# Performance work log

Measured on AMD Instinct MI355X. Metric: run time of the kernel, lower is better.

## Reference

```python
import jax, jax.numpy as jnp
import numpy as np

B, N = 8, 512
EMBED, EDGE_D, FLAG_D = 256, 32, 32
NODE_NUM, EDGE_NUM, FLAG_NUM = 20000, 16, 4
IN_DIM = 2 * EMBED + 2 * FLAG_D + EDGE_D  # concat order: [head_emb, tail_emb, head_flag, tail_flag, edge]
NEG = -1e12


def setup_inputs() -> dict:
    key = jax.random.key(0)
    ks = jax.random.split(key, 16)
    s = 0.05
    return {
        "adjacent_matrix": jax.random.randint(ks[0], (B, N, N), 0, 2, dtype=jnp.int32),
        "head_nodes": jax.random.randint(ks[1], (B, N), 0, NODE_NUM, dtype=jnp.int32),
        "head_flag_bit_matrix": jax.random.randint(ks[2], (B, N), 0, FLAG_NUM, dtype=jnp.int32),
        "edge_type_matrix": jax.random.randint(ks[3], (B, N, N), 0, EDGE_NUM, dtype=jnp.int32),
        "node_emb": jax.random.normal(ks[4], (NODE_NUM, EMBED)) * s,
        "edge_emb": jax.random.normal(ks[5], (EDGE_NUM, EDGE_D)) * s,
        "flag_emb": jax.random.normal(ks[6], (FLAG_NUM, FLAG_D)) * s,
        "t1_w": jax.random.normal(ks[7], (EMBED, EMBED)) * s,
        "t1_b": jax.random.normal(ks[8], (EMBED,)) * s,
        "w1": jax.random.normal(ks[9], (IN_DIM,)) * s,
        "b1": jax.random.normal(ks[10], ()) * s,
        "t2_w": jax.random.normal(ks[11], (EMBED, EMBED)) * s,
        "t2_b": jax.random.normal(ks[12], (EMBED,)) * s,
        "w2": jax.random.normal(ks[13], (IN_DIM,)) * s,
        "b2": jax.random.normal(ks[14], ()) * s,
    }


def _leaky_relu(x):
    return jnp.where(x > 0, x, 0.1 * x)


def _gat_layer(h, f, e, adj, w, b):
    # Decompose Linear(concat([h_i, h_j, f_i, f_j, e_ij])) into per-part dot
    # products summed by broadcasting -> avoids the [B,N,N,IN_DIM] concat.
    D, F = h.shape[-1], f.shape[-1]
    wh, wt = w[:D], w[D:2 * D]
    wfh, wft = w[2 * D:2 * D + F], w[2 * D + F:2 * D + 2 * F]
    we = w[2 * D + 2 * F:]
    logit = ((h @ wh)[:, :, None] + (h @ wt)[:, None, :]
             + (f @ wfh)[:, :, None] + (f @ wft)[:, None, :]
             + jnp.einsum('bije,e->bij', e, we) + b)  # [B,N,N]
    logit = _leaky_relu(logit)
    logit = jnp.where(adj == 0, NEG, logit)
    att = jax.nn.softmax(logit, axis=1)  # softmax over head axis i
    # out[b,j] = sum_i att[b,i,j] * h[b,i]   (== bmm(att^T, h))
    return jnp.einsum('bij,bid->bjd', att, h)


def reference(adjacent_matrix, head_nodes, head_flag_bit_matrix, edge_type_matrix,
              node_emb, edge_emb, flag_emb,
              t1_w, t1_b, w1, b1, t2_w, t2_b, w2, b2):
    h = node_emb[head_nodes] @ t1_w.T + t1_b          # [B,N,D] (t1 projection)
    f = flag_emb[head_flag_bit_matrix]                # [B,N,F]
    e = edge_emb[edge_type_matrix]                    # [B,N,N,E]
    t = _gat_layer(h, f, e, adjacent_matrix, w1, b1)  # layer 1 aggregate
    t = jax.nn.sigmoid(t)
    h2 = t @ t2_w.T + t2_b                            # t2 projection
    return _gat_layer(h2, f, e, adjacent_matrix, w2, b2)
```

## Files before the change

### kernel.cpp

```cpp
#include <hip/hip_runtime.h>
#include <hip/hip_bf16.h>

#define BB 8
#define NN 512
#define DD 256
#define NROWS (BB*NN)
#define JT 16

using bf16x8 = __attribute__((ext_vector_type(8))) short;
using f32x4  = __attribute__((ext_vector_type(4))) float;
typedef unsigned short us_t;

__device__ __forceinline__ us_t f2bf(float x) {
    union { float f; unsigned int u; } v; v.f = x;
    unsigned int r = (v.u + 0x7fffu + ((v.u >> 16) & 1u)) >> 16;
    return (us_t)r;
}

__global__ __launch_bounds__(256) void k1(
    const float* __restrict__ w1f, const float* __restrict__ bias1,
    const float* __restrict__ node_emb, const int* __restrict__ head_nodes,
    const float* __restrict__ wvec1, const int* __restrict__ flagidx,
    const float* __restrict__ flag_emb,
    us_t* __restrict__ hT, float* __restrict__ a1, float* __restrict__ c1,
    const float* __restrict__ w2f, us_t* __restrict__ Wb2,
    const int* __restrict__ adj, const int* __restrict__ et,
    unsigned char* __restrict__ pk)
{
    __shared__ float redA[64], redC[64];
    const int blk = blockIdx.x, t = threadIdx.x;

    if (blk >= 320) {
        int pb = blk - 320;
        int pbid = ((pb & 7) << 8) | (pb >> 3);
        int g = (pbid*256 + t)*4;
        int4 av = *(const int4*)(adj + g);
        int4 ev = *(const int4*)(et + g);
        uchar4 u;
        u.x = (unsigned char)((ev.x&15)|(av.x<<4));
        u.y = (unsigned char)((ev.y&15)|(av.y<<4));
        u.z = (unsigned char)((ev.z&15)|(av.z<<4));
        u.w = (unsigned char)((ev.w&15)|(av.w<<4));
        *(uchar4*)(pk + g) = u;
        return;
    }
    if (blk >= 256) {
        int i = (blk - 256)*1024 + t*4;
        float4 wv = *(const float4*)(w2f + i);
        ushort4 u;
        u.x = f2bf(wv.x); u.y = f2bf(wv.y); u.z = f2bf(wv.z); u.w = f2bf(wv.w);
        *(ushort4*)&Wb2[i] = u;
        return;
    }

    const int bid = ((blk & 7) << 5) | (blk >> 3);
    const int wave = t >> 6, lane = t & 63;
    const int lrow = lane & 15, kg = lane >> 4;
    const int r0 = bid * 16;
    const int dw = wave * 64;

    const int arow = r0 + lrow;
    const int nid = head_nodes[arow];

    f32x4 acc[4];
    #pragma unroll
    for (int n = 0; n < 4; ++n) acc[n] = (f32x4){0.f, 0.f, 0.f, 0.f};

    const float4* xr = (const float4*)(node_emb + (size_t)nid * DD);
    #pragma unroll
    for (int ks = 0; ks < DD/32; ++ks) {
        float4 xa = xr[ks*8 + kg*2];
        float4 xb = xr[ks*8 + kg*2 + 1];
        bf16x8 af;
        af[0] = (short)f2bf(xa.x); af[1] = (short)f2bf(xa.y);
        af[2] = (short)f2bf(xa.z); af[3] = (short)f2bf(xa.w);
        af[4] = (short)f2bf(xb.x); af[5] = (short)f2bf(xb.y);
        af[6] = (short)f2bf(xb.z); af[7] = (short)f2bf(xb.w);
        #pragma unroll
        for (int n = 0; n < 4; ++n) {
            const float4* wr = (const float4*)(w1f + (size_t)(dw + n*16 + lrow)*DD
                                                + ks*32 + kg*8);
            float4 wa = wr[0], wb = wr[1];
            bf16x8 bfr;
            bfr[0] = (short)f2bf(wa.x); bfr[1] = (short)f2bf(wa.y);
            bfr[2] = (short)f2bf(wa.z); bfr[3] = (short)f2bf(wa.w);
            bfr[4] = (short)f2bf(wb.x); bfr[5] = (short)f2bf(wb.y);
            bfr[6] = (short)f2bf(wb.z); bfr[7] = (short)f2bf(wb.w);
            acc[n] = __builtin_amdgcn_mfma_f32_16x16x32_bf16(af, bfr, acc[n], 0, 0, 0);
        }
    }

    const int b  = r0 >> 9;
    const int i0 = (r0 & 511) + kg*4;
    float pa[4] = {0.f,0.f,0.f,0.f}, pc[4] = {0.f,0.f,0.f,0.f};
    #pragma unroll
    for (int n = 0; n < 4; ++n) {
        int d = dw + n*16 + lrow;
        float bv = bias1[d];
        float whd = wvec1[d], wtd = wvec1[256+d];
        ushort4 u;
        #pragma unroll
        for (int r = 0; r < 4; ++r) {
            float v = acc[n][r] + bv;
            ((us_t*)&u)[r] = f2bf(v);
            pa[r] += v * whd;
            pc[r] += v * wtd;
        }
        *(ushort4*)&hT[(size_t)b*DD*NN + (size_t)d*NN + i0] = u;
    }
    #pragma unroll
    for (int r = 0; r < 4; ++r) {
        #pragma unroll
        for (int m = 1; m < 16; m <<= 1) {
            pa[r] += __shfl_xor(pa[r], m);
            pc[r] += __shfl_xor(pc[r], m);
        }
    }
    if (lrow == 0) {
        #pragma unroll
        for (int r = 0; r < 4; ++r) {
            redA[wave*16 + kg*4 + r] = pa[r];
            redC[wave*16 + kg*4 + r] = pc[r];
        }
    }
    __syncthreads();
    if (t < 128) {
        const int m = t >> 3, sub = t & 7;
        const int fi = flagidx[r0 + m];
        float fa = 0.f, fc = 0.f;
        #pragma unroll
        for (int q = 0; q < 4; ++q) {
            int e = sub*4 + q;
            float fe = flag_emb[fi*32 + e];
            fa += fe * wvec1[512 + e];
            fc += fe * wvec1[544 + e];
        }
        #pragma unroll
        for (int mm = 1; mm < 8; mm <<= 1) {
            fa += __shfl_xor(fa, mm);
            fc += __shfl_xor(fc, mm);
        }
        if (sub == 0) {
            float sa = fa, sc = fc;
            #pragma unroll
            for (int wv = 0; wv < 4; ++wv) { sa += redA[wv*16 + m]; sc += redC[wv*16 + m]; }
            a1[r0 + m] = sa;
            c1[r0 + m] = sc;
        }
    }
}

__global__ __launch_bounds__(512) void attn1_lin2(
    const unsigned char* __restrict__ pk,
    const float* __restrict__ edge_emb, const float* __restrict__ w,
    const float* __restrict__ bptr,
    const float* __restrict__ a, const float* __restrict__ c,
    const us_t* __restrict__ hT,
    const us_t* __restrict__ Wb2, const float* __restrict__ bias2,
    const float* __restrict__ wvec2, const int* __restrict__ flagidx,
    const float* __restrict__ flag_emb,
    us_t* __restrict__ hT2, float* __restrict__ a2, float* __restrict__ c2)
{
    __shared__ __align__(16) float p[NN][JT+1];
    __shared__ __align__(16) us_t Pb[JT][NN+8];
    __shared__ __align__(16) us_t Sg[16][DD+8];
    __shared__ float as[NN];
    __shared__ float edot[16];
    __shared__ float cjs[JT];
    __shared__ float redw[8][16];
    __shared__ float mj[JT];
    __shared__ float invden[JT];
    __shared__ float redA[128], redC[128];

    const int t = threadIdx.x;
    const int b  = blockIdx.x & 7;
    const int j0 = (blockIdx.x >> 3) * JT;
    const int wave = t >> 6, lane = t & 63;

    as[t] = a[b*NN + t];
    if (t < 16) {
        float s = 0.f;
        for (int e2 = 0; e2 < 32; ++e2)
            s += edge_emb[t*32 + e2] * w[576 + e2];
        edot[t] = s;
    } else if (t < 32) {
        cjs[t-16] = c[b*NN + j0 + (t-16)];
    }
    const float bias = bptr[0];
    __syncthreads();

    const unsigned char* pkb = pk + (size_t)b*NN*NN + j0;
    #pragma unroll
    for (int it = 0; it < 4; ++it) {
        int lid4 = (it*512 + t) * 4;
        int i = lid4 >> 4, jj = lid4 & 15;
        uchar4 u = *(const uchar4*)(pkb + (size_t)i*NN + jj);
        float base = as[i] + bias;
        unsigned char uv[4] = {u.x, u.y, u.z, u.w};
        #pragma unroll
        for (int q = 0; q < 4; ++q) {
            float l = base + cjs[jj+q] + edot[uv[q] & 15];
            l = (l > 0.f) ? l : 0.1f*l;
            p[i][jj+q] = (uv[q] >> 4) ? l : -1.0e30f;
        }
    }
    __syncthreads();

    const int j = t & 15, grp = t >> 4;
    float lv[16];
    #pragma unroll
    for (int s = 0; s < 16; ++s) lv[s] = p[grp + s*32][j];
    float m = lv[0];
    #pragma unroll
    for (int s = 1; s < 16; ++s) m = fmaxf(m, lv[s]);
    m = fmaxf(m, __shfl_xor(m, 16));
    m = fmaxf(m, __shfl_xor(m, 32));
    if (lane < 16) redw[wave][lane] = m;
    __syncthreads();
    if (t < 16) {
        float mm = redw[0][t];
        #pragma unroll
        for (int wv = 1; wv < 8; ++wv) mm = fmaxf(mm, redw[wv][t]);
        mj[t] = mm;
    }
    __syncthreads();
    const float mmax = mj[j];
    float ssum = 0.f;
    #pragma unroll
    for (int s = 0; s < 16; ++s) {
        float v = __expf(lv[s] - mmax);
        Pb[j][grp + s*32] = f2bf(v);
        ssum += v;
    }
    ssum += __shfl_xor(ssum, 16);
    ssum += __shfl_xor(ssum, 32);
    if (lane < 16) redw[wave][lane] = ssum;
    __syncthreads();
    if (t < 16) {
        float sm = redw[0][t];
        #pragma unroll
        for (int wv = 1; wv < 8; ++wv) sm += redw[wv][t];
        invden[t] = 1.f / sm;
    }
    __syncthreads();

    const int dw = wave * 32;
    const int lrow = lane & 15;
    const int kg   = lane >> 4;
    f32x4 acc[2];
    acc[0] = (f32x4){0.f,0.f,0.f,0.f};
    acc[1] = (f32x4){0.f,0.f,0.f,0.f};

    const us_t* hTb = hT + (size_t)b*DD*NN;
    const us_t* hp[2];
    hp[0] = hTb + (size_t)(dw + lrow)*NN + kg*8;
    hp[1] = hTb + (size_t)(dw + 16 + lrow)*NN + kg*8;

    #pragma unroll 4
    for (int ks = 0; ks < NN/32; ++ks) {
        int k0 = ks*32;
        bf16x8 afr = *(const bf16x8*)&Pb[lrow][kg*8 + k0];
        #pragma unroll
        for (int n = 0; n < 2; ++n) {
            bf16x8 bfr = *(const bf16x8*)(hp[n] + k0);
            acc[n] = __builtin_amdgcn_mfma_f32_16x16x32_bf16(afr, bfr, acc[n], 0, 0, 0);
        }
    }

    float idr[4];
    #pragma unroll
    for (int r = 0; r < 4; ++r) idr[r] = invden[kg*4 + r];
    #pragma unroll
    for (int n = 0; n < 2; ++n) {
        #pragma unroll
        for (int r = 0; r < 4; ++r) {
            float v = 1.f/(1.f + __expf(-acc[n][r]*idr[r]));
            Sg[kg*4 + r][dw + n*16 + lrow] = f2bf(v);
        }
    }
    __syncthreads();

    f32x4 acc2[2];
    acc2[0] = (f32x4){0.f,0.f,0.f,0.f};
    acc2[1] = (f32x4){0.f,0.f,0.f,0.f};
    #pragma unroll
    for (int ks = 0; ks < DD/32; ++ks) {
        bf16x8 af2 = *(const bf16x8*)&Sg[lrow][ks*32 + kg*8];
        #pragma unroll
        for (int n = 0; n < 2; ++n) {
            bf16x8 bf2 = *(const bf16x8*)(Wb2 + (size_t)(dw + n*16 + lrow)*DD
                                           + ks*32 + kg*8);
            acc2[n] = __builtin_amdgcn_mfma_f32_16x16x32_bf16(af2, bf2, acc2[n], 0, 0, 0);
        }
    }

    const int r0 = b*NN + j0;
    const int i0 = j0 + kg*4;
    float pa[4] = {0.f,0.f,0.f,0.f}, pc[4] = {0.f,0.f,0.f,0.f};
    #pragma unroll
    for (int n = 0; n < 2; ++n) {
        int d = dw + n*16 + lrow;
        float bv = bias2[d];
        float whd = wvec2[d], wtd = wvec2[256+d];
        ushort4 u;
        #pragma unroll
        for (int r = 0; r < 4; ++r) {
            float v = acc2[n][r] + bv;
            ((us_t*)&u)[r] = f2bf(v);
            pa[r] += v * whd;
            pc[r] += v * wtd;
        }
        *(ushort4*)&hT2[(size_t)b*DD*NN + (size_t)d*NN + i0] = u;
    }
    #pragma unroll
    for (int r = 0; r < 4; ++r) {
        #pragma unroll
        for (int mk = 1; mk < 16; mk <<= 1) {
            pa[r] += __shfl_xor(pa[r], mk);
            pc[r] += __shfl_xor(pc[r], mk);
        }
    }
    if (lrow == 0) {
        #pragma unroll
        for (int r = 0; r < 4; ++r) {
            redA[wave*16 + kg*4 + r] = pa[r];
            redC[wave*16 + kg*4 + r] = pc[r];
        }
    }
    __syncthreads();
    if (t < 128) {
        const int mrow = t >> 3, sub = t & 7;
        const int fi = flagidx[r0 + mrow];
        float fa = 0.f, fc = 0.f;
        #pragma unroll
        for (int q = 0; q < 4; ++q) {
            int e = sub*4 + q;
            float fe = flag_emb[fi*32 + e];
            fa += fe * wvec2[512 + e];
            fc += fe * wvec2[544 + e];
        }
        #pragma unroll
        for (int mm = 1; mm < 8; mm <<= 1) {
            fa += __shfl_xor(fa, mm);
            fc += __shfl_xor(fc, mm);
        }
        if (sub == 0) {
            float sa = fa, sc = fc;
            #pragma unroll
            for (int wv = 0; wv < 8; ++wv) { sa += redA[wv*16 + mrow]; sc += redC[wv*16 + mrow]; }
            a2[r0 + mrow] = sa;
            c2[r0 + mrow] = sc;
        }
    }
}

__global__ __launch_bounds__(512) void attn2(
    const unsigned char* __restrict__ pk,
    const float* __restrict__ edge_emb, const float* __restrict__ w,
    const float* __restrict__ bptr,
    const float* __restrict__ a, const float* __restrict__ c,
    const us_t* __restrict__ hT,
    float* __restrict__ outf)
{
    __shared__ __align__(16) float p[NN][JT+1];
    __shared__ __align__(16) us_t Pb[JT][NN+8];
    __shared__ float as[NN];
    __shared__ float edot[16];
    __shared__ float cjs[JT];
    __shared__ float redw[8][16];
    __shared__ float mj[JT];
    __shared__ float invden[JT];

    const int t = threadIdx.x;
    const int b  = blockIdx.x & 7;
    const int j0 = (blockIdx.x >> 3) * JT;
    const int wave = t >> 6, lane = t & 63;

    as[t] = a[b*NN + t];
    if (t < 16) {
        float s = 0.f;
        for (int e2 = 0; e2 < 32; ++e2)
            s += edge_emb[t*32 + e2] * w[576 + e2];
        edot[t] = s;
    } else if (t < 32) {
        cjs[t-16] = c[b*NN + j0 + (t-16)];
    }
    const float bias = bptr[0];
    __syncthreads();

    const unsigned char* pkb = pk + (size_t)b*NN*NN + j0;
    #pragma unroll
    for (int it = 0; it < 4; ++it) {
        int lid4 = (it*512 + t) * 4;
        int i = lid4 >> 4, jj = lid4 & 15;
        uchar4 u = *(const uchar4*)(pkb + (size_t)i*NN + jj);
        float base = as[i] + bias;
        unsigned char uv[4] = {u.x, u.y, u.z, u.w};
        #pragma unroll
        for (int q = 0; q < 4; ++q) {
            float l = base + cjs[jj+q] + edot[uv[q] & 15];
            l = (l > 0.f) ? l : 0.1f*l;
            p[i][jj+q] = (uv[q] >> 4) ? l : -1.0e30f;
        }
    }
    __syncthreads();

    const int j = t & 15, grp = t >> 4;
    float lv[16];
    #pragma unroll
    for (int s = 0; s < 16; ++s) lv[s] = p[grp + s*32][j];
    float m = lv[0];
    #pragma unroll
    for (int s = 1; s < 16; ++s) m = fmaxf(m, lv[s]);
    m = fmaxf(m, __shfl_xor(m, 16));
    m = fmaxf(m, __shfl_xor(m, 32));
    if (lane < 16) redw[wave][lane] = m;
    __syncthreads();
    if (t < 16) {
        float mm = redw[0][t];
        #pragma unroll
        for (int wv = 1; wv < 8; ++wv) mm = fmaxf(mm, redw[wv][t]);
        mj[t] = mm;
    }
    __syncthreads();
    const float mmax = mj[j];
    float ssum = 0.f;
    #pragma unroll
    for (int s = 0; s < 16; ++s) {
        float v = __expf(lv[s] - mmax);
        Pb[j][grp + s*32] = f2bf(v);
        ssum += v;
    }
    ssum += __shfl_xor(ssum, 16);
    ssum += __shfl_xor(ssum, 32);
    if (lane < 16) redw[wave][lane] = ssum;
    __syncthreads();
    if (t < 16) {
        float sm = redw[0][t];
        #pragma unroll
        for (int wv = 1; wv < 8; ++wv) sm += redw[wv][t];
        invden[t] = 1.f / sm;
    }
    __syncthreads();

    const int dw = wave * 32;
    const int lrow = lane & 15;
    const int kg   = lane >> 4;
    f32x4 acc[2];
    acc[0] = (f32x4){0.f,0.f,0.f,0.f};
    acc[1] = (f32x4){0.f,0.f,0.f,0.f};

    const us_t* hTb = hT + (size_t)b*DD*NN;
    const us_t* hp[2];
    hp[0] = hTb + (size_t)(dw + lrow)*NN + kg*8;
    hp[1] = hTb + (size_t)(dw + 16 + lrow)*NN + kg*8;

    #pragma unroll 4
    for (int ks = 0; ks < NN/32; ++ks) {
        int k0 = ks*32;
        bf16x8 afr = *(const bf16x8*)&Pb[lrow][kg*8 + k0];
        #pragma unroll
        for (int n = 0; n < 2; ++n) {
            bf16x8 bfr = *(const bf16x8*)(hp[n] + k0);
            acc[n] = __builtin_amdgcn_mfma_f32_16x16x32_bf16(afr, bfr, acc[n], 0, 0, 0);
        }
    }

    float idr[4];
    #pragma unroll
    for (int r = 0; r < 4; ++r) idr[r] = invden[kg*4 + r];
    #pragma unroll
    for (int n = 0; n < 2; ++n) {
        #pragma unroll
        for (int r = 0; r < 4; ++r) {
            int jj = j0 + kg*4 + r;
            int dd = dw + n*16 + lrow;
            outf[(size_t)(b*NN + jj)*DD + dd] = acc[n][r] * idr[r];
        }
    }
}

extern "C" void kernel_launch(void* const* d_in, const int* in_sizes, int n_in,
                              void* d_out, int out_size, void* d_ws, size_t ws_size,
                              hipStream_t stream) {
    (void)in_sizes; (void)n_in; (void)out_size; (void)ws_size;
    const int*   adj       = (const int*)d_in[0];
    const int*   head_nodes= (const int*)d_in[1];
    const int*   head_flag = (const int*)d_in[2];
    const int*   etype     = (const int*)d_in[3];
    const float* node_emb  = (const float*)d_in[4];
    const float* edge_emb  = (const float*)d_in[5];
    const float* flag_emb  = (const float*)d_in[6];
    const float* t1_w      = (const float*)d_in[7];
    const float* t1_b      = (const float*)d_in[8];
    const float* w1        = (const float*)d_in[9];
    const float* b1        = (const float*)d_in[10];
    const float* t2_w      = (const float*)d_in[11];
    const float* t2_b      = (const float*)d_in[12];
    const float* w2        = (const float*)d_in[13];
    const float* b2        = (const float*)d_in[14];

    us_t* hT1 = (us_t*)d_ws;
    us_t* hT2 = hT1 + (size_t)NROWS*DD;
    us_t* Wb2 = hT2 + (size_t)NROWS*DD;
    unsigned char* pk = (unsigned char*)(Wb2 + (size_t)DD*DD);
    float* a1 = (float*)(pk + (size_t)BB*NN*NN);
    float* c1 = a1 + NROWS;
    float* a2 = c1 + NROWS;
    float* c2 = a2 + NROWS;

    k1<<<320 + BB*NN*NN/1024, 256, 0, stream>>>(
        t1_w, t1_b, node_emb, head_nodes, w1, head_flag, flag_emb,
        hT1, a1, c1, t2_w, Wb2, adj, etype, pk);
    attn1_lin2<<<BB*(NN/JT), 512, 0, stream>>>(
        pk, edge_emb, w1, b1, a1, c1, hT1,
        Wb2, t2_b, w2, head_flag, flag_emb, hT2, a2, c2);
    attn2<<<BB*(NN/JT), 512, 0, stream>>>(
        pk, edge_emb, w2, b2, a2, c2, hT2, (float*)d_out);
}
```

Measured before the change: 46.35 us.

## Fuse both attention layers into one cooperative kernel with per-batch barrier

Merges the two attention kernels into a single cooperatively launched kernel. Blocks of the same batch synchronize through an atomic counter that k1 zeroes, replacing the kernel boundary between layer 1 and layer 2. This removes one launch gap and its tail, at the cost of spin-waiting and the need for all 256 blocks to be co-resident.

```diff
diff --git a/kernel.cpp b/kernel.cpp
--- a/kernel.cpp
+++ b/kernel.cpp
@@ -25,7 +25,7 @@
     us_t* __restrict__ hT, float* __restrict__ a1, float* __restrict__ c1,
     const float* __restrict__ w2f, us_t* __restrict__ Wb2,
     const int* __restrict__ adj, const int* __restrict__ et,
-    unsigned char* __restrict__ pk)
+    unsigned char* __restrict__ pk, int* __restrict__ ctr)
 {
     __shared__ float redA[64], redC[64];
     const int blk = blockIdx.x, t = threadIdx.x;
@@ -45,6 +45,7 @@
         return;
     }
     if (blk >= 256) {
+        if (blk == 256 && t < BB) ctr[t] = 0;
         int i = (blk - 256)*1024 + t*4;
         float4 wv = *(const float4*)(w2f + i);
         ushort4 u;
@@ -150,16 +151,20 @@
     }
 }
 
-__global__ __launch_bounds__(512) void attn1_lin2(
-    const unsigned char* __restrict__ pk,
-    const float* __restrict__ edge_emb, const float* __restrict__ w,
-    const float* __restrict__ bptr,
-    const float* __restrict__ a, const float* __restrict__ c,
-    const us_t* __restrict__ hT,
-    const us_t* __restrict__ Wb2, const float* __restrict__ bias2,
-    const float* __restrict__ wvec2, const int* __restrict__ flagidx,
-    const float* __restrict__ flag_emb,
-    us_t* __restrict__ hT2, float* __restrict__ a2, float* __restrict__ c2)
+struct AttnParams {
+    const unsigned char* pk;
+    const float *edge_emb;
+    const float *w1, *b1, *a1, *c1;
+    const us_t  *hT1;
+    const us_t  *Wb2; const float *bias2;
+    const float *w2;  const int *flagidx; const float *flag_emb;
+    us_t *hT2; float *a2; float *c2;
+    const float *b2;
+    float *outf;
+    int *ctr;
+};
+
+__global__ __launch_bounds__(512) void attn_fused(AttnParams P)
 {
     __shared__ __align__(16) float p[NN][JT+1];
     __shared__ __align__(16) us_t Pb[JT][NN+8];
@@ -176,306 +181,295 @@
     const int b  = blockIdx.x & 7;
     const int j0 = (blockIdx.x >> 3) * JT;
     const int wave = t >> 6, lane = t & 63;
-
-    as[t] = a[b*NN + t];
-    if (t < 16) {
-        float s = 0.f;
-        for (int e2 = 0; e2 < 32; ++e2)
-            s += edge_emb[t*32 + e2] * w[576 + e2];
-        edot[t] = s;
-    } else if (t < 32) {
-        cjs[t-16] = c[b*NN + j0 + (t-16)];
-    }
-    const float bias = bptr[0];
+    const int lrow = lane & 15, kg = lane >> 4;
+
+    {
+        as[t] = P.a1[b*NN + t];
+        if (t < 16) {
+            float s = 0.f;
+            for (int e2 = 0; e2 < 32; ++e2)
+                s += P.edge_emb[t*32 + e2] * P.w1[576 + e2];
+            edot[t] = s;
+        } else if (t < 32) {
+            cjs[t-16] = P.c1[b*NN + j0 + (t-16)];
+        }
+        const float bias = P.b1[0];
+        __syncthreads();
+
+        const unsigned char* pkb = P.pk + (size_t)b*NN*NN + j0;
+        #pragma unroll
+        for (int it = 0; it < 4; ++it) {
+            int lid4 = (it*512 + t) * 4;
+            int i = lid4 >> 4, jj = lid4 & 15;
+            uchar4 u = *(const uchar4*)(pkb + (size_t)i*NN + jj);
+            float base = as[i] + bias;
+            unsigned char uv[4] = {u.x, u.y, u.z, u.w};
+            #pragma unroll
+            for (int q = 0; q < 4; ++q) {
+                float l = base + cjs[jj+q] + edot[uv[q] & 15];
+                l = (l > 0.f) ? l : 0.1f*l;
+                p[i][jj+q] = (uv[q] >> 4) ? l : -1.0e30f;
+            }
+        }
+        __syncthreads();
+
+        const int j = t & 15, grp = t >> 4;
+        float lv[16];
+        #pragma unroll
+        for (int s = 0; s < 16; ++s) lv[s] = p[grp + s*32][j];
+        float m = lv[0];
+        #pragma unroll
+        for (int s = 1; s < 16; ++s) m = fmaxf(m, lv[s]);
+        m = fmaxf(m, __shfl_xor(m, 16));
+        m = fmaxf(m, __shfl_xor(m, 32));
+        if (lane < 16) redw[wave][lane] = m;
+        __syncthreads();
+        if (t < 16) {
+            float mm = redw[0][t];
+            #pragma unroll
+            for (int wv = 1; wv < 8; ++wv) mm = fmaxf(mm, redw[wv][t]);
+            mj[t] = mm;
+        }
+        __syncthreads();
+        const float mmax = mj[j];
+        float ssum = 0.f;
+        #pragma unroll
+        for (int s = 0; s < 16; ++s) {
+            float v = __expf(lv[s] - mmax);
+            Pb[j][grp + s*32] = f2bf(v);
+            ssum += v;
+        }
+        ssum += __shfl_xor(ssum, 16);
+        ssum += __shfl_xor(ssum, 32);
+        if (lane < 16) redw[wave][lane] = ssum;
+        __syncthreads();
+        if (t < 16) {
+            float sm = redw[0][t];
+            #pragma unroll
+            for (int wv = 1; wv < 8; ++wv) sm += redw[wv][t];
+            invden[t] = 1.f / sm;
+        }
+        __syncthreads();
+
+        const int dw = wave * 32;
+        f32x4 acc[2];
+        acc[0] = (f32x4){0.f,0.f,0.f,0.f};
+        acc[1] = (f32x4){0.f,0.f,0.f,0.f};
+
+        const us_t* hTb = P.hT1 + (size_t)b*DD*NN;
+        const us_t* hp[2];
+        hp[0] = hTb + (size_t)(dw + lrow)*NN + kg*8;
+        hp[1] = hTb + (size_t)(dw + 16 + lrow)*NN + kg*8;
+
+        #pragma unroll 4
+        for (int ks = 0; ks < NN/32; ++ks) {
+            int k0 = ks*32;
+            bf16x8 afr = *(const bf16x8*)&Pb[lrow][kg*8 + k0];
+            #pragma unroll
+            for (int n = 0; n < 2; ++n) {
+                bf16x8 bfr = *(const bf16x8*)(hp[n] + k0);
+                acc[n] = __builtin_amdgcn_mfma_f32_16x16x32_bf16(afr, bfr, acc[n], 0, 0, 0);
+            }
+        }
+
+        float idr[4];
+        #pragma unroll
+        for (int r = 0; r < 4; ++r) idr[r] = invden[kg*4 + r];
+        #pragma unroll
+        for (int n = 0; n < 2; ++n) {
+            #pragma unroll
+            for (int r = 0; r < 4; ++r) {
+                float v = 1.f/(1.f + __expf(-acc[n][r]*idr[r]));
+                Sg[kg*4 + r][dw + n*16 + lrow] = f2bf(v);
+            }
+        }
+        __syncthreads();
+
+        f32x4 acc2[2];
+        acc2[0] = (f32x4){0.f,0.f,0.f,0.f};
+        acc2[1] = (f32x4){0.f,0.f,0.f,0.f};
+        #pragma unroll
+        for (int ks = 0; ks < DD/32; ++ks) {
+            bf16x8 af2 = *(const bf16x8*)&Sg[lrow][ks*32 + kg*8];
+            #pragma unroll
+            for (int n = 0; n < 2; ++n) {
+                bf16x8 bf2 = *(const bf16x8*)(P.Wb2 + (size_t)(dw + n*16 + lrow)*DD
+                                               + ks*32 + kg*8);
+                acc2[n] = __builtin_amdgcn_mfma_f32_16x16x32_bf16(af2, bf2, acc2[n], 0, 0, 0);
+            }
+        }
+
+        const int r0 = b*NN + j0;
+        const int i0 = j0 + kg*4;
+        float pa[4] = {0.f,0.f,0.f,0.f}, pc[4] = {0.f,0.f,0.f,0.f};
+        #pragma unroll
+        for (int n = 0; n < 2; ++n) {
+            int d = dw + n*16 + lrow;
+            float bv = P.bias2[d];
+            float whd = P.w2[d], wtd = P.w2[256+d];
+            ushort4 u;
+            #pragma unroll
+            for (int r = 0; r < 4; ++r) {
+                float v = acc2[n][r] + bv;
+                ((us_t*)&u)[r] = f2bf(v);
+                pa[r] += v * whd;
+                pc[r] += v * wtd;
+            }
+            *(ushort4*)&P.hT2[(size_t)b*DD*NN + (size_t)d*NN + i0] = u;
+        }
+        #pragma unroll
+        for (int r = 0; r < 4; ++r) {
+            #pragma unroll
+            for (int mk = 1; mk < 16; mk <<= 1) {
+                pa[r] += __shfl_xor(pa[r], mk);
+                pc[r] += __shfl_xor(pc[r], mk);
+            }
+        }
+        if (lrow == 0) {
+            #pragma unroll
+            for (int r = 0; r < 4; ++r) {
+                redA[wave*16 + kg*4 + r] = pa[r];
+                redC[wave*16 + kg*4 + r] = pc[r];
+            }
+        }
+        __syncthreads();
+        if (t < 128) {
+            const int mrow = t >> 3, sub = t & 7;
+            const int fi = P.flagidx[r0 + mrow];
+            float fa = 0.f, fc = 0.f;
+            #pragma unroll
+            for (int q = 0; q < 4; ++q) {
+                int e = sub*4 + q;
+                float fe = P.flag_emb[fi*32 + e];
+                fa += fe * P.w2[512 + e];
+                fc += fe * P.w2[544 + e];
+            }
+            #pragma unroll
+            for (int mm = 1; mm < 8; mm <<= 1) {
+                fa += __shfl_xor(fa, mm);
+                fc += __shfl_xor(fc, mm);
+            }
+            if (sub == 0) {
+                float sa = fa, sc = fc;
+                #pragma unroll
+                for (int wv = 0; wv < 8; ++wv) { sa += redA[wv*16 + mrow]; sc += redC[wv*16 + mrow]; }
+                P.a2[r0 + mrow] = sa;
+                P.c2[r0 + mrow] = sc;
+            }
+        }
+    }
+
     __syncthreads();
-
-    const unsigned char* pkb = pk + (size_t)b*NN*NN + j0;
-    #pragma unroll
-    for (int it = 0; it < 4; ++it) {
-        int lid4 = (it*512 + t) * 4;
-        int i = lid4 >> 4, jj = lid4 & 15;
-        uchar4 u = *(const uchar4*)(pkb + (size_t)i*NN + jj);
-        float base = as[i] + bias;
-        unsigned char uv[4] = {u.x, u.y, u.z, u.w};
-        #pragma unroll
-        for (int q = 0; q < 4; ++q) {
-            float l = base + cjs[jj+q] + edot[uv[q] & 15];
-            l = (l > 0.f) ? l : 0.1f*l;
-            p[i][jj+q] = (uv[q] >> 4) ? l : -1.0e30f;
-        }
-    }
+    __threadfence();
     __syncthreads();
-
-    const int j = t & 15, grp = t >> 4;
-    float lv[16];
-    #pragma unroll
-    for (int s = 0; s < 16; ++s) lv[s] = p[grp + s*32][j];
-    float m = lv[0];
-    #pragma unroll
-    for (int s = 1; s < 16; ++s) m = fmaxf(m, lv[s]);
-    m = fmaxf(m, __shfl_xor(m, 16));
-    m = fmaxf(m, __shfl_xor(m, 32));
-    if (lane < 16) redw[wave][lane] = m;
+    if (t == 0) {
+        atomicAdd(P.ctr + b, 1);
+        while (__hip_atomic_load(P.ctr + b, __ATOMIC_ACQUIRE,
+                                 __HIP_MEMORY_SCOPE_AGENT) < 32) {}
+    }
     __syncthreads();
-    if (t < 16) {
-        float mm = redw[0][t];
-        #pragma unroll
-        for (int wv = 1; wv < 8; ++wv) mm = fmaxf(mm, redw[wv][t]);
-        mj[t] = mm;
-    }
-    __syncthreads();
-    const float mmax = mj[j];
-    float ssum = 0.f;
-    #pragma unroll
-    for (int s = 0; s < 16; ++s) {
-        float v = __expf(lv[s] - mmax);
-        Pb[j][grp + s*32] = f2bf(v);
-        ssum += v;
-    }
-    ssum += __shfl_xor(ssum, 16);
-    ssum += __shfl_xor(ssum, 32);
-    if (lane < 16) redw[wave][lane] = ssum;
-    __syncthreads();
-    if (t < 16) {
-        float sm = redw[0][t];
-        #pragma unroll
-        for (int wv = 1; wv < 8; ++wv) sm += redw[wv][t];
-        invden[t] = 1.f / sm;
-    }
-    __syncthreads();
-
-    const int dw = wave * 32;
-    const int lrow = lane & 15;
-    const int kg   = lane >> 4;
-    f32x4 acc[2];
-    acc[0] = (f32x4){0.f,0.f,0.f,0.f};
-    acc[1] = (f32x4){0.f,0.f,0.f,0.f};
-
-    const us_t* hTb = hT + (size_t)b*DD*NN;
-    const us_t* hp[2];
-    hp[0] = hTb + (size_t)(dw + lrow)*NN + kg*8;
-    hp[1] = hTb + (size_t)(dw + 16 + lrow)*NN + kg*8;
-
-    #pragma unroll 4
-    for (int ks = 0; ks < NN/32; ++ks) {
-        int k0 = ks*32;
-        bf16x8 afr = *(const bf16x8*)&Pb[lrow][kg*8 + k0];
+    __threadfence();
+
+    {
+        as[t] = P.a2[b*NN + t];
+        if (t < 16) {
+            float s = 0.f;
+            for (int e2 = 0; e2 < 32; ++e2)
+                s += P.edge_emb[t*32 + e2] * P.w2[576 + e2];
+            edot[t] = s;
+        } else if (t < 32) {
+            cjs[t-16] = P.c2[b*NN + j0 + (t-16)];
+        }
+        const float bias = P.b2[0];
+        __syncthreads();
+
+        const unsigned char* pkb = P.pk + (size_t)b*NN*NN + j0;
+        #pragma unroll
+        for (int it = 0; it < 4; ++it) {
+            int lid4 = (it*512 + t) * 4;
+            int i = lid4 >> 4, jj = lid4 & 15;
+            uchar4 u = *(const uchar4*)(pkb + (size_t)i*NN + jj);
+            float base = as[i] + bias;
+            unsigned char uv[4] = {u.x, u.y, u.z, u.w};
+            #pragma unroll
+            for (int q = 0; q < 4; ++q) {
+                float l = base + cjs[jj+q] + edot[uv[q] & 15];
+                l = (l > 0.f) ? l : 0.1f*l;
+                p[i][jj+q] = (uv[q] >> 4) ? l : -1.0e30f;
+            }
+        }
+        __syncthreads();
+
+        const int j = t & 15, grp = t >> 4;
+        float lv[16];
+        #pragma unroll
+        for (int s = 0; s < 16; ++s) lv[s] = p[grp + s*32][j];
+        float m = lv[0];
+        #pragma unroll
+        for (int s = 1; s < 16; ++s) m = fmaxf(m, lv[s]);
+        m = fmaxf(m, __shfl_xor(m, 16));
+        m = fmaxf(m, __shfl_xor(m, 32));
+        if (lane < 16) redw[wave][lane] = m;
+        __syncthreads();
+        if (t < 16) {
+            float mm = redw[0][t];
+            #pragma unroll
+            for (int wv = 1; wv < 8; ++wv) mm = fmaxf(mm, redw[wv][t]);
+            mj[t] = mm;
+        }
+        __syncthreads();
+        const float mmax = mj[j];
+        float ssum = 0.f;
+        #pragma unroll
+        for (int s = 0; s < 16; ++s) {
+            float v = __expf(lv[s] - mmax);
+            Pb[j][grp + s*32] = f2bf(v);
+            ssum += v;
+        }
+        ssum += __shfl_xor(ssum, 16);
+        ssum += __shfl_xor(ssum, 32);
+        if (lane < 16) redw[wave][lane] = ssum;
+        __syncthreads();
+        if (t < 16) {
+            float sm = redw[0][t];
+            #pragma unroll
+            for (int wv = 1; wv < 8; ++wv) sm += redw[wv][t];
+            invden[t] = 1.f / sm;
+        }
+        __syncthreads();
+
+        const int dw = wave * 32;
+        f32x4 acc[2];
+        acc[0] = (f32x4){0.f,0.f,0.f,0.f};
+        acc[1] = (f32x4){0.f,0.f,0.f,0.f};
+
+        const us_t* hTb = P.hT2 + (size_t)b*DD*NN;
+        const us_t* hp[2];
+        hp[0] = hTb + (size_t)(dw + lrow)*NN + kg*8;
+        hp[1] = hTb + (size_t)(dw + 16 + lrow)*NN + kg*8;
+
+        #pragma unroll 4
+        for (int ks = 0; ks < NN/32; ++ks) {
+            int k0 = ks*32;
+            bf16x8 afr = *(const bf16x8*)&Pb[lrow][kg*8 + k0];
+            #pragma unroll
+            for (int n = 0; n < 2; ++n) {
+                bf16x8 bfr = *(const bf16x8*)(hp[n] + k0);
+                acc[n] = __builtin_amdgcn_mfma_f32_16x16x32_bf16(afr, bfr, acc[n], 0, 0, 0);
+            }
+        }
+
+        float idr[4];
+        #pragma unroll
+        for (int r = 0; r < 4; ++r) idr[r] = invden[kg*4 + r];
         #pragma unroll
         for (int n = 0; n < 2; ++n) {
-            bf16x8 bfr = *(const bf16x8*)(hp[n] + k0);
-            acc[n] = __builtin_amdgcn_mfma_f32_16x16x32_bf16(afr, bfr, acc[n], 0, 0, 0);
-        }
-    }
-
-    float idr[4];
-    #pragma unroll
-    for (int r = 0; r < 4; ++r) idr[r] = invden[kg*4 + r];
-    #pragma unroll
-    for (int n = 0; n < 2; ++n) {
-        #pragma unroll
-        for (int r = 0; r < 4; ++r) {
-            float v = 1.f/(1.f + __expf(-acc[n][r]*idr[r]));
-            Sg[kg*4 + r][dw + n*16 + lrow] = f2bf(v);
-        }
-    }
-    __syncthreads();
-
-    f32x4 acc2[2];
-    acc2[0] = (f32x4){0.f,0.f,0.f,0.f};
-    acc2[1] = (f32x4){0.f,0.f,0.f,0.f};
-    #pragma unroll
-    for (int ks = 0; ks < DD/32; ++ks) {
-        bf16x8 af2 = *(const bf16x8*)&Sg[lrow][ks*32 + kg*8];
-        #pragma unroll
-        for (int n = 0; n < 2; ++n) {
-            bf16x8 bf2 = *(const bf16x8*)(Wb2 + (size_t)(dw + n*16 + lrow)*DD
-                                           + ks*32 + kg*8);
-            acc2[n] = __builtin_amdgcn_mfma_f32_16x16x32_bf16(af2, bf2, acc2[n], 0, 0, 0);
-        }
-    }
-
-    const int r0 = b*NN + j0;
-    const int i0 = j0 + kg*4;
-    float pa[4] = {0.f,0.f,0.f,0.f}, pc[4] = {0.f,0.f,0.f,0.f};
-    #pragma unroll
-    for (int n = 0; n < 2; ++n) {
-        int d = dw + n*16 + lrow;
-        float bv = bias2[d];
-        float whd = wvec2[d], wtd = wvec2[256+d];
-        ushort4 u;
-        #pragma unroll
-        for (int r = 0; r < 4; ++r) {
-            float v = acc2[n][r] + bv;
-            ((us_t*)&u)[r] = f2bf(v);
-            pa[r] += v * whd;
-            pc[r] += v * wtd;
-        }
-        *(ushort4*)&hT2[(size_t)b*DD*NN + (size_t)d*NN + i0] = u;
-    }
-    #pragma unroll
-    for (int r = 0; r < 4; ++r) {
-        #pragma unroll
-        for (int mk = 1; mk < 16; mk <<= 1) {
-            pa[r] += __shfl_xor(pa[r], mk);
-            pc[r] += __shfl_xor(pc[r], mk);
-        }
-    }
-    if (lrow == 0) {
-        #pragma unroll
-        for (int r = 0; r < 4; ++r) {
-            redA[wave*16 + kg*4 + r] = pa[r];
-            redC[wave*16 + kg*4 + r] = pc[r];
-        }
-    }
-    __syncthreads();
-    if (t < 128) {
-        const int mrow = t >> 3, sub = t & 7;
-        const int fi = flagidx[r0 + mrow];
-        float fa = 0.f, fc = 0.f;
-        #pragma unroll
-        for (int q = 0; q < 4; ++q) {
-            int e = sub*4 + q;
-            float fe = flag_emb[fi*32 + e];
-            fa += fe * wvec2[512 + e];
-            fc += fe * wvec2[544 + e];
-        }
-        #pragma unroll
-        for (int mm = 1; mm < 8; mm <<= 1) {
-            fa += __shfl_xor(fa, mm);
-            fc += __shfl_xor(fc, mm);
-        }
-        if (sub == 0) {
-            float sa = fa, sc = fc;
-            #pragma unroll
-            for (int wv = 0; wv < 8; ++wv) { sa += redA[wv*16 + mrow]; sc += redC[wv*16 + mrow]; }
-            a2[r0 + mrow] = sa;
-            c2[r0 + mrow] = sc;
-        }
-    }
-}
-
-__global__ __launch_bounds__(512) void attn2(
-    const unsigned char* __restrict__ pk,
-    const float* __restrict__ edge_emb, const float* __restrict__ w,
-    const float* __restrict__ bptr,
-    const float* __restrict__ a, const float* __restrict__ c,
-    const us_t* __restrict__ hT,
-    float* __restrict__ outf)
-{
-    __shared__ __align__(16) float p[NN][JT+1];
-    __shared__ __align__(16) us_t Pb[JT][NN+8];
-    __shared__ float as[NN];
-    __shared__ float edot[16];
-    __shared__ float cjs[JT];
-    __shared__ float redw[8][16];
-    __shared__ float mj[JT];
-    __shared__ float invden[JT];
-
-    const int t = threadIdx.x;
-    const int b  = blockIdx.x & 7;
-    const int j0 = (blockIdx.x >> 3) * JT;
-    const int wave = t >> 6, lane = t & 63;
-
-    as[t] = a[b*NN + t];
-    if (t < 16) {
-        float s = 0.f;
-        for (int e2 = 0; e2 < 32; ++e2)
-            s += edge_emb[t*32 + e2] * w[576 + e2];
-        edot[t] = s;
-    } else if (t < 32) {
-        cjs[t-16] = c[b*NN + j0 + (t-16)];
-    }
-    const float bias = bptr[0];
-    __syncthreads();
-
-    const unsigned char* pkb = pk + (size_t)b*NN*NN + j0;
-    #pragma unroll
-    for (int it = 0; it < 4; ++it) {
-        int lid4 = (it*512 + t) * 4;
-        int i = lid4 >> 4, jj = lid4 & 15;
-        uchar4 u = *(const uchar4*)(pkb + (size_t)i*NN + jj);
-        float base = as[i] + bias;
-        unsigned char uv[4] = {u.x, u.y, u.z, u.w};
-        #pragma unroll
-        for (int q = 0; q < 4; ++q) {
-            float l = base + cjs[jj+q] + edot[uv[q] & 15];
-            l = (l > 0.f) ? l : 0.1f*l;
-            p[i][jj+q] = (uv[q] >> 4) ? l : -1.0e30f;
-        }
-    }
-    __syncthreads();
-
-    const int j = t & 15, grp = t >> 4;
-    float lv[16];
-    #pragma unroll
-    for (int s = 0; s < 16; ++s) lv[s] = p[grp + s*32][j];
-    float m = lv[0];
-    #pragma unroll
-    for (int s = 1; s < 16; ++s) m = fmaxf(m, lv[s]);
-    m = fmaxf(m, __shfl_xor(m, 16));
-    m = fmaxf(m, __shfl_xor(m, 32));
-    if (lane < 16) redw[wave][lane] = m;
-    __syncthreads();
-    if (t < 16) {
-        float mm = redw[0][t];
-        #pragma unroll
-        for (int wv = 1; wv < 8; ++wv) mm = fmaxf(mm, redw[wv][t]);
-        mj[t] = mm;
-    }
-    __syncthreads();
-    const float mmax = mj[j];
-    float ssum = 0.f;
-    #pragma unroll
-    for (int s = 0; s < 16; ++s) {
-        float v = __expf(lv[s] - mmax);
-        Pb[j][grp + s*32] = f2bf(v);
-        ssum += v;
-    }
-    ssum += __shfl_xor(ssum, 16);
-    ssum += __shfl_xor(ssum, 32);
-    if (lane < 16) redw[wave][lane] = ssum;
-    __syncthreads();
-    if (t < 16) {
-        float sm = redw[0][t];
-        #pragma unroll
-        for (int wv = 1; wv < 8; ++wv) sm += redw[wv][t];
-        invden[t] = 1.f / sm;
-    }
-    __syncthreads();
-
-    const int dw = wave * 32;
-    const int lrow = lane & 15;
-    const int kg   = lane >> 4;
-    f32x4 acc[2];
-    acc[0] = (f32x4){0.f,0.f,0.f,0.f};
-    acc[1] = (f32x4){0.f,0.f,0.f,0.f};
-
-    const us_t* hTb = hT + (size_t)b*DD*NN;
-    const us_t* hp[2];
-    hp[0] = hTb + (size_t)(dw + lrow)*NN + kg*8;
-    hp[1] = hTb + (size_t)(dw + 16 + lrow)*NN + kg*8;
-
-    #pragma unroll 4
-    for (int ks = 0; ks < NN/32; ++ks) {
-        int k0 = ks*32;
-        bf16x8 afr = *(const bf16x8*)&Pb[lrow][kg*8 + k0];
-        #pragma unroll
-        for (int n = 0; n < 2; ++n) {
-            bf16x8 bfr = *(const bf16x8*)(hp[n] + k0);
-            acc[n] = __builtin_amdgcn_mfma_f32_16x16x32_bf16(afr, bfr, acc[n], 0, 0, 0);
-        }
-    }
-
-    float idr[4];
-    #pragma unroll
-    for (int r = 0; r < 4; ++r) idr[r] = invden[kg*4 + r];
-    #pragma unroll
-    for (int n = 0; n < 2; ++n) {
-        #pragma unroll
-        for (int r = 0; r < 4; ++r) {
-            int jj = j0 + kg*4 + r;
-            int dd = dw + n*16 + lrow;
-            outf[(size_t)(b*NN + jj)*DD + dd] = acc[n][r] * idr[r];
+            #pragma unroll
+            for (int r = 0; r < 4; ++r) {
+                int jj = j0 + kg*4 + r;
+                int dd = dw + n*16 + lrow;
+                P.outf[(size_t)(b*NN + jj)*DD + dd] = acc[n][r] * idr[r];
+            }
         }
     }
 }
@@ -508,13 +502,24 @@
     float* c1 = a1 + NROWS;
     float* a2 = c1 + NROWS;
     float* c2 = a2 + NROWS;
+    int*   ctr = (int*)(c2 + NROWS);
 
     k1<<<320 + BB*NN*NN/1024, 256, 0, stream>>>(
         t1_w, t1_b, node_emb, head_nodes, w1, head_flag, flag_emb,
-        hT1, a1, c1, t2_w, Wb2, adj, etype, pk);
-    attn1_lin2<<<BB*(NN/JT), 512, 0, stream>>>(
-        pk, edge_emb, w1, b1, a1, c1, hT1,
-        Wb2, t2_b, w2, head_flag, flag_emb, hT2, a2, c2);
-    attn2<<<BB*(NN/JT), 512, 0, stream>>>(
-        pk, edge_emb, w2, b2, a2, c2, hT2, (float*)d_out);
+        hT1, a1, c1, t2_w, Wb2, adj, etype, pk, ctr);
+
+    AttnParams P;
+    P.pk = pk; P.edge_emb = edge_emb;
+    P.w1 = w1; P.b1 = b1; P.a1 = a1; P.c1 = c1;
+    P.hT1 = hT1;
+    P.Wb2 = Wb2; P.bias2 = t2_b;
+    P.w2 = w2; P.flagidx = head_flag; P.flag_emb = flag_emb;
+    P.hT2 = hT2; P.a2 = a2; P.c2 = c2;
+    P.b2 = b2;
+    P.outf = (float*)d_out;
+    P.ctr = ctr;
+
+    void* args[] = { &P };
+    hipLaunchCooperativeKernel((const void*)attn_fused, dim3(BB*(NN/JT)),
+                               dim3(512), args, 0, stream);
 }
```

Measured after the change: 133.4 us. +187.9%, slower.
